# Performance work log

Hardware: AMD Instinct MI355X
Metric: run time of the kernel (lower is better)

Reference implementation:

```python
import jax, jax.numpy as jnp
import numpy as np

INPUT_SIZE = 1024
OUTPUT_SIZE = 15
EXPERT_NUM = 10
BS = 65536


def setup_inputs() -> dict:
    key = jax.random.key(0)
    k1, k2, k3, k4, k5 = jax.random.split(key, 5)
    bound = 1.0 / np.sqrt(INPUT_SIZE)
    x = jax.random.normal(k1, (BS, INPUT_SIZE), dtype=jnp.float32)
    expert_w = jax.random.uniform(k2, (EXPERT_NUM, OUTPUT_SIZE, INPUT_SIZE), minval=-bound, maxval=bound, dtype=jnp.float32)
    expert_b = jax.random.uniform(k3, (EXPERT_NUM, OUTPUT_SIZE), minval=-bound, maxval=bound, dtype=jnp.float32)
    gate_w = jax.random.uniform(k4, (EXPERT_NUM, OUTPUT_SIZE, INPUT_SIZE), minval=-bound, maxval=bound, dtype=jnp.float32)
    gate_b = jax.random.uniform(k5, (EXPERT_NUM, OUTPUT_SIZE), minval=-bound, maxval=bound, dtype=jnp.float32)
    return {"x": x, "expert_w": expert_w, "expert_b": expert_b, "gate_w": gate_w, "gate_b": gate_b}


def reference(x, expert_w, expert_b, gate_w, gate_b):
    # miu, xi: (bs, out, E) -- matches torch.stack(..., dim=-1)
    miu = jnp.einsum('bi,eoi->boe', x, expert_w) + expert_b.T[None]  # (bs, out, E)
    xi = jnp.einsum('bi,eoi->boe', x, gate_w) + gate_b.T[None]       # (bs, out, E)
    g = jax.nn.softmax(xi, axis=-1)                                  # softmax over experts
    return jnp.sum(g * miu, axis=-1)                                 # (bs, out)
```

## Files before the change

kernel.cpp:

```cpp
#include <hip/hip_runtime.h>

#define KDIM 1024
#define NOUT 15
#define NEXP 10
#define BM   64
#define NKS  32
#define QPT  20
#define SCOL 305

typedef short bf16x8 __attribute__((ext_vector_type(8)));
typedef float f32x16 __attribute__((ext_vector_type(16)));

__device__ __forceinline__ unsigned f2bf2(float a, float b) {
    unsigned ua = __float_as_uint(a);
    unsigned ub = __float_as_uint(b);
    ua = (ua + 0x7FFFu + ((ua >> 16) & 1u)) >> 16;
    ub = (ub + 0x7FFFu + ((ub >> 16) & 1u)) & 0xFFFF0000u;
    return ua | ub;
}

__global__ void wconv_kernel(const float* __restrict__ ew,
                             const float* __restrict__ gw,
                             unsigned short* __restrict__ ws)
{
    int U  = blockIdx.x * 256 + threadIdx.x;
    int L  = U & 63;
    int q  = (U >> 6) % QPT;
    int ks = U / (QPT * 64);
    int nt = q >> 1, kt = q & 1;
    int wrow = nt * 32 + (L & 31);
    int wcol = ks * 32 + kt * 16 + (L >> 5) * 8;
    float4 a = {0.f,0.f,0.f,0.f}, b = {0.f,0.f,0.f,0.f};
    if (wrow < 150) {
        a = *(const float4*)(ew + wrow * KDIM + wcol);
        b = *(const float4*)(ew + wrow * KDIM + wcol + 4);
    } else if (wrow < 300) {
        a = *(const float4*)(gw + (wrow - 150) * KDIM + wcol);
        b = *(const float4*)(gw + (wrow - 150) * KDIM + wcol + 4);
    }
    uint4 o;
    o.x = f2bf2(a.x, a.y); o.y = f2bf2(a.z, a.w);
    o.z = f2bf2(b.x, b.y); o.w = f2bf2(b.z, b.w);
    *(uint4*)(ws + (size_t)U * 8) = o;
}

__global__ void __launch_bounds__(256, 3)
moe_kernel(const float* __restrict__ x,
           const unsigned short* __restrict__ wsrc,
           const float* __restrict__ eb,
           const float* __restrict__ gb,
           float* __restrict__ out)
{
    __shared__ float ep[32][SCOL];

    const int tid = threadIdx.x;
    const int wv  = tid >> 6;
    const int L   = tid & 63;
    const int mw  = wv >> 1;
    const int nw  = wv & 1;
    const int ln  = L & 31;
    const int lh  = L >> 5;

    const float* xrow = x + ((size_t)blockIdx.x * BM + mw * 32 + ln) * KDIM + lh * 8;
    const bf16x8* wf = (const bf16x8*)wsrc + L;

    f32x16 acc[5];
    #pragma unroll
    for (int nt = 0; nt < 5; ++nt)
        #pragma unroll
        for (int r = 0; r < 16; ++r)
            acc[nt][r] = 0.f;

    float4 xa[2][2];
    #pragma unroll
    for (int kt = 0; kt < 2; ++kt) {
        xa[kt][0] = *(const float4*)(xrow + kt * 16);
        xa[kt][1] = *(const float4*)(xrow + kt * 16 + 4);
    }

    #pragma unroll 2
    for (int ks = 0; ks < NKS; ++ks) {
        float4 xn[2][2];
        if (ks + 1 < NKS) {
            #pragma unroll
            for (int kt = 0; kt < 2; ++kt) {
                xn[kt][0] = *(const float4*)(xrow + (ks + 1) * 32 + kt * 16);
                xn[kt][1] = *(const float4*)(xrow + (ks + 1) * 32 + kt * 16 + 4);
            }
        }

        bf16x8 af[2];
        #pragma unroll
        for (int kt = 0; kt < 2; ++kt) {
            union { unsigned u[4]; bf16x8 v; } pk;
            pk.u[0] = f2bf2(xa[kt][0].x, xa[kt][0].y);
            pk.u[1] = f2bf2(xa[kt][0].z, xa[kt][0].w);
            pk.u[2] = f2bf2(xa[kt][1].x, xa[kt][1].y);
            pk.u[3] = f2bf2(xa[kt][1].z, xa[kt][1].w);
            af[kt] = pk.v;
        }

        #pragma unroll
        for (int nt = 0; nt < 5; ++nt) {
            #pragma unroll
            for (int kt = 0; kt < 2; ++kt) {
                int q = (nw * 5 + nt) * 2 + kt;
                bf16x8 bf = wf[((size_t)ks * QPT + q) * 64];
                acc[nt] = __builtin_amdgcn_mfma_f32_32x32x16_bf16(af[kt], bf, acc[nt], 0, 0, 0);
            }
        }

        #pragma unroll
        for (int kt = 0; kt < 2; ++kt) {
            xa[kt][0] = xn[kt][0];
            xa[kt][1] = xn[kt][1];
        }
    }

    #pragma unroll 1
    for (int g = 0; g < 2; ++g) {
        if (mw == g) {
            #pragma unroll
            for (int nt = 0; nt < 5; ++nt) {
                int col = nw * 160 + nt * 32 + ln;
                if (col < 300) {
                    #pragma unroll
                    for (int r = 0; r < 16; ++r)
                        ep[(r & 3) + 8 * (r >> 2) + 4 * lh][col] = acc[nt][r];
                }
            }
        }
        __syncthreads();

        #pragma unroll 1
        for (int t = tid; t < 32 * NOUT; t += 256) {
            int row = t / NOUT, o = t % NOUT;
            float xi[NEXP], miu_v[NEXP];
            float mx = -1e30f;
            #pragma unroll
            for (int e = 0; e < NEXP; ++e) {
                miu_v[e] = ep[row][e * NOUT + o]       + eb[e * NOUT + o];
                xi[e]    = ep[row][150 + e * NOUT + o] + gb[e * NOUT + o];
                mx = fmaxf(mx, xi[e]);
            }
            float s = 0.f, v = 0.f;
            #pragma unroll
            for (int e = 0; e < NEXP; ++e) {
                float g2 = __expf(xi[e] - mx);
                s += g2;
                v += g2 * miu_v[e];
            }
            out[((size_t)blockIdx.x * BM + g * 32 + row) * NOUT + o] = v / s;
        }
        __syncthreads();
    }
}

extern "C" void kernel_launch(void* const* d_in, const int* in_sizes, int n_in,
                              void* d_out, int out_size, void* d_ws, size_t ws_size,
                              hipStream_t stream) {
    const float* x  = (const float*)d_in[0];
    const float* ew = (const float*)d_in[1];
    const float* eb = (const float*)d_in[2];
    const float* gw = (const float*)d_in[3];
    const float* gb = (const float*)d_in[4];
    float* out = (float*)d_out;
    unsigned short* ws = (unsigned short*)d_ws;

    wconv_kernel<<<160, 256, 0, stream>>>(ew, gw, ws);
    moe_kernel<<<65536 / BM, 256, 0, stream>>>(x, ws, eb, gb, out);
}
```

Baseline: 446.7 us.

## Stage x through double-buffered swizzled LDS with coalesced loads and shared bf16 conversion

Rather than each wave loading its own strided 32-byte slices of x from global memory, the block now loads 128-column chunks of x with coalesced float4 reads. It converts them to bf16 once and writes them into double-buffered, XOR-swizzled LDS that overlays the epilogue buffer. Each wave then reads its MFMA A fragments from LDS, with the next chunk's global loads kept in flight across a manual barrier that uses a vmcnt wait. This targets poorly coalesced global access and the duplicate loading and conversion of x by the two N-waves. In exchange it adds LDS traffic, per-chunk barriers and more registers, which could cut occupancy.

```diff
diff --git a/kernel.cpp b/kernel.cpp
--- a/kernel.cpp
+++ b/kernel.cpp
@@ -4,7 +4,7 @@
 #define NOUT 15
 #define NEXP 10
 #define BM   64
-#define NKS  32
+#define NCH  8
 #define QPT  20
 #define SCOL 305
 
@@ -17,6 +17,13 @@
     ua = (ua + 0x7FFFu + ((ua >> 16) & 1u)) >> 16;
     ub = (ub + 0x7FFFu + ((ub >> 16) & 1u)) & 0xFFFF0000u;
     return ua | ub;
+}
+
+__device__ __forceinline__ void kbar8() {
+    __builtin_amdgcn_sched_barrier(0);
+    asm volatile("s_waitcnt vmcnt(8) lgkmcnt(0)" ::: "memory");
+    __builtin_amdgcn_s_barrier();
+    __builtin_amdgcn_sched_barrier(0);
 }
 
 __global__ void wconv_kernel(const float* __restrict__ ew,
@@ -51,7 +58,10 @@
            const float* __restrict__ gb,
            float* __restrict__ out)
 {
-    __shared__ float ep[32][SCOL];
+    __shared__ union {
+        unsigned short xs[2][8192];
+        float ep[32][SCOL];
+    } sm;
 
     const int tid = threadIdx.x;
     const int wv  = tid >> 6;
@@ -61,8 +71,14 @@
     const int ln  = L & 31;
     const int lh  = L >> 5;
 
-    const float* xrow = x + ((size_t)blockIdx.x * BM + mw * 32 + ln) * KDIM + lh * 8;
-    const bf16x8* wf = (const bf16x8*)wsrc + L;
+    const int sro = 2 * (wv * 8) + lh;
+    const int sc  = (L & 31) * 4;
+    const int skq = (L & 31) >> 1;
+    const int sh8 = ((L & 31) & 1) * 8;
+
+    const float* xgb = x + (size_t)blockIdx.x * BM * KDIM;
+    const bf16x8* wfL = (const bf16x8*)wsrc + L;
+    const int arow = mw * 32 + ln;
 
     f32x16 acc[5];
     #pragma unroll
@@ -71,50 +87,56 @@
         for (int r = 0; r < 16; ++r)
             acc[nt][r] = 0.f;
 
-    float4 xa[2][2];
-    #pragma unroll
-    for (int kt = 0; kt < 2; ++kt) {
-        xa[kt][0] = *(const float4*)(xrow + kt * 16);
-        xa[kt][1] = *(const float4*)(xrow + kt * 16 + 4);
-    }
+    float4 xr[8];
 
-    #pragma unroll 2
-    for (int ks = 0; ks < NKS; ++ks) {
-        float4 xn[2][2];
-        if (ks + 1 < NKS) {
+    auto xload = [&](int ch) {
+        #pragma unroll
+        for (int j = 0; j < 8; ++j)
+            xr[j] = *(const float4*)(xgb + (size_t)(sro + 2 * j) * KDIM + ch * 128 + sc);
+    };
+    auto xwriteb = [&](unsigned short* xbuf) {
+        #pragma unroll
+        for (int j = 0; j < 8; ++j) {
+            int r = sro + 2 * j;
+            int unit = skq * 64 + (r ^ (skq & 7));
+            uint2 o;
+            o.x = f2bf2(xr[j].x, xr[j].y);
+            o.y = f2bf2(xr[j].z, xr[j].w);
+            *(uint2*)((char*)xbuf + unit * 16 + sh8) = o;
+        }
+    };
+    auto computec = [&](int ch, const unsigned short* xbuf) {
+        #pragma unroll
+        for (int sl = 0; sl < 4; ++sl) {
+            const int kq0 = sl * 4 + lh;
+            const int kq1 = sl * 4 + 2 + lh;
+            bf16x8 af0 = *(const bf16x8*)((const char*)xbuf + (kq0 * 64 + (arow ^ (kq0 & 7))) * 16);
+            bf16x8 af1 = *(const bf16x8*)((const char*)xbuf + (kq1 * 64 + (arow ^ (kq1 & 7))) * 16);
+            const int ks = ch * 4 + sl;
             #pragma unroll
-            for (int kt = 0; kt < 2; ++kt) {
-                xn[kt][0] = *(const float4*)(xrow + (ks + 1) * 32 + kt * 16);
-                xn[kt][1] = *(const float4*)(xrow + (ks + 1) * 32 + kt * 16 + 4);
+            for (int nt = 0; nt < 5; ++nt) {
+                const int q = (nw * 5 + nt) * 2;
+                bf16x8 b0 = wfL[(size_t)(ks * QPT + q) * 64];
+                bf16x8 b1 = wfL[(size_t)(ks * QPT + q + 1) * 64];
+                acc[nt] = __builtin_amdgcn_mfma_f32_32x32x16_bf16(af0, b0, acc[nt], 0, 0, 0);
+                acc[nt] = __builtin_amdgcn_mfma_f32_32x32x16_bf16(af1, b1, acc[nt], 0, 0, 0);
             }
         }
+    };
 
-        bf16x8 af[2];
-        #pragma unroll
-        for (int kt = 0; kt < 2; ++kt) {
-            union { unsigned u[4]; bf16x8 v; } pk;
-            pk.u[0] = f2bf2(xa[kt][0].x, xa[kt][0].y);
-            pk.u[1] = f2bf2(xa[kt][0].z, xa[kt][0].w);
-            pk.u[2] = f2bf2(xa[kt][1].x, xa[kt][1].y);
-            pk.u[3] = f2bf2(xa[kt][1].z, xa[kt][1].w);
-            af[kt] = pk.v;
+    xload(0);
+    xwriteb(sm.xs[0]);
+    xload(1);
+    kbar8();
+
+    #pragma unroll 1
+    for (int ch = 0; ch < NCH; ++ch) {
+        computec(ch, sm.xs[ch & 1]);
+        if (ch + 1 < NCH) {
+            xwriteb(sm.xs[(ch + 1) & 1]);
+            if (ch + 2 < NCH) xload(ch + 2);
         }
-
-        #pragma unroll
-        for (int nt = 0; nt < 5; ++nt) {
-            #pragma unroll
-            for (int kt = 0; kt < 2; ++kt) {
-                int q = (nw * 5 + nt) * 2 + kt;
-                bf16x8 bf = wf[((size_t)ks * QPT + q) * 64];
-                acc[nt] = __builtin_amdgcn_mfma_f32_32x32x16_bf16(af[kt], bf, acc[nt], 0, 0, 0);
-            }
-        }
-
-        #pragma unroll
-        for (int kt = 0; kt < 2; ++kt) {
-            xa[kt][0] = xn[kt][0];
-            xa[kt][1] = xn[kt][1];
-        }
+        kbar8();
     }
 
     #pragma unroll 1
@@ -126,7 +148,7 @@
                 if (col < 300) {
                     #pragma unroll
                     for (int r = 0; r < 16; ++r)
-                        ep[(r & 3) + 8 * (r >> 2) + 4 * lh][col] = acc[nt][r];
+                        sm.ep[(r & 3) + 8 * (r >> 2) + 4 * lh][col] = acc[nt][r];
                 }
             }
         }
@@ -139,8 +161,8 @@
             float mx = -1e30f;
             #pragma unroll
             for (int e = 0; e < NEXP; ++e) {
-                miu_v[e] = ep[row][e * NOUT + o]       + eb[e * NOUT + o];
-                xi[e]    = ep[row][150 + e * NOUT + o] + gb[e * NOUT + o];
+                miu_v[e] = sm.ep[row][e * NOUT + o]       + eb[e * NOUT + o];
+                xi[e]    = sm.ep[row][150 + e * NOUT + o] + gb[e * NOUT + o];
                 mx = fmaxf(mx, xi[e]);
             }
             float s = 0.f, v = 0.f;
```

Measured after the change: 458.4 us. 2.6% more time.
